# Performance work log

Hardware: AMD Instinct MI355X
Metric: run time of the kernel (lower is better)

The kernel has to match this reference:

```python
import jax, jax.numpy as jnp
import numpy as np
import math

B, L, HID = 2, 2048, 1024
H, DK, RATIO, SHARED, TOPK = 4, 64, 4, 1, 2
EXP_V = 2
DV = DK * EXP_V
KEY_DIM = H * DK
VAL_DIM = KEY_DIM * EXP_V
HE = H * RATIO
KS = 4
EPS = 1e-5


def _silu(x):
    return x * jax.nn.sigmoid(x)


def _dwconv_causal(x, w):
    # x: (B, L, C), w: (C, KS); causal depthwise short conv
    xp = jnp.pad(x, ((0, 0), (KS - 1, 0), (0, 0))).transpose(0, 2, 1)
    y = jax.lax.conv_general_dilated(xp, w[:, None, :], (1,), 'VALID',
                                     feature_group_count=w.shape[0],
                                     dimension_numbers=('NCH', 'OIH', 'NCH'))
    return y.transpose(0, 2, 1)


def _l2norm(x):
    return x * jax.lax.rsqrt(jnp.sum(x * x, -1, keepdims=True) + 1e-6)


def _forward(hidden_states, Wq, Wk, Wv, Wb, Wa, Wg, Wo, conv_q, conv_k, conv_v,
             Wq_exp, Wk_exp, W_gate, A_log, dt_bias, norm_w):
    x = hidden_states
    q = _silu(_dwconv_causal(x @ Wq.T, conv_q)).reshape(B, L, H, DK)
    k = _silu(_dwconv_causal(x @ Wk.T, conv_k)).reshape(B, L, H, DK)
    v = _silu(_dwconv_causal(x @ Wv.T, conv_v)).reshape(B, L, H, DV)
    # per-head expert expansion -> (B,L,H,RATIO,DK)
    qe = jnp.einsum('blhd,hkd->blhk', q, Wq_exp).reshape(B, L, H, RATIO, DK)
    ke = jnp.einsum('blhd,hkd->blhk', k, Wk_exp).reshape(B, L, H, RATIO, DK)
    qe = _l2norm(qe) * (DK ** -0.5)
    ke = _l2norm(ke)
    # token-policy top-k routing over non-shared experts
    logits = jnp.einsum('blhd,nd->blhn', q, W_gate)
    scores = jax.nn.softmax(logits.astype(jnp.float32), axis=-1)
    tw, ti = jax.lax.top_k(scores, TOPK)
    tw = tw / jnp.sum(tw, -1, keepdims=True)
    full = jnp.sum(jax.nn.one_hot(ti + SHARED, RATIO, dtype=tw.dtype) * tw[..., None], axis=-2)
    full = full.at[..., :SHARED].set(1.0 / SHARED)
    w_r = (full / jnp.sum(full, -1, keepdims=True)).astype(x.dtype)  # (B,L,H,RATIO)
    mask = (w_r > 0).astype(x.dtype)
    beta = jax.nn.sigmoid(x @ Wb.T).reshape(B, L, H, RATIO) * mask
    g = -jnp.exp(A_log).reshape(H, RATIO) * jax.nn.softplus((x @ Wa.T) + dt_bias).reshape(B, L, H, RATIO)
    g = g * mask  # unrouted memories: exp(0)=1, no decay, no update
    # gated delta-rule recurrence over HE = H*RATIO memories
    qs = qe.reshape(B, L, HE, DK).transpose(1, 0, 2, 3)
    ks_ = ke.reshape(B, L, HE, DK).transpose(1, 0, 2, 3)
    vs = jnp.broadcast_to(v[:, :, :, None, :], (B, L, H, RATIO, DV)).reshape(B, L, HE, DV).transpose(1, 0, 2, 3)
    bs = beta.reshape(B, L, HE).transpose(1, 0, 2)
    gs = g.reshape(B, L, HE).transpose(1, 0, 2)

    def step(S, xs):
        qt, kt, vt, bt, gt = xs
        S = S * jnp.exp(gt)[..., None, None]
        kv = jnp.einsum('bhk,bhkv->bhv', kt, S)
        S = S + jnp.einsum('bhk,bhv->bhkv', kt, (vt - kv) * bt[..., None])
        return S, jnp.einsum('bhk,bhkv->bhv', qt, S)

    S0 = jnp.zeros((B, HE, DK, DV), x.dtype)
    _, o = jax.lax.scan(step, S0, (qs, ks_, vs, bs, gs))
    o = o.transpose(1, 0, 2, 3).reshape(B, L, H, RATIO, DV)
    o = jnp.einsum('blhe,blhev->blhv', w_r, o)
    # FusedRMSNormSwishGate + output projection
    gate = (x @ Wg.T).reshape(B, L, H, DV)
    o = o * jax.lax.rsqrt(jnp.mean(o * o, -1, keepdims=True) + EPS) * norm_w * _silu(gate)
    return o.reshape(B, L, VAL_DIM) @ Wo.T


def setup_inputs():
    keys = jax.random.split(jax.random.key(0), 18)
    n = lambda i, shp, sc=1.0: jax.random.normal(keys[i], shp, jnp.float32) * sc
    A = jax.random.uniform(keys[14], (HE,), jnp.float32, 1e-3, 16.0)
    dt = jnp.exp(jax.random.uniform(keys[15], (HE,), jnp.float32) * (math.log(0.1) - math.log(0.001)) + math.log(0.001))
    dt = jnp.clip(dt, 1e-4, None)
    return {
        'hidden_states': n(0, (B, L, HID)),
        'Wq': n(1, (KEY_DIM, HID), HID ** -0.5),
        'Wk': n(2, (KEY_DIM, HID), HID ** -0.5),
        'Wv': n(3, (VAL_DIM, HID), HID ** -0.5),
        'Wb': n(4, (HE, HID), HID ** -0.5),
        'Wa': n(5, (HE, HID), HID ** -0.5),
        'Wg': n(6, (VAL_DIM, HID), HID ** -0.5),
        'Wo': n(7, (HID, VAL_DIM), VAL_DIM ** -0.5),
        'conv_q': n(8, (KEY_DIM, KS), 0.5),
        'conv_k': n(9, (KEY_DIM, KS), 0.5),
        'conv_v': n(10, (VAL_DIM, KS), 0.5),
        'Wq_exp': n(11, (H, RATIO * DK, DK), DK ** -0.5),
        'Wk_exp': n(12, (H, RATIO * DK, DK), DK ** -0.5),
        'W_gate': n(13, (RATIO - SHARED, DK), DK ** -0.5),
        'A_log': jnp.log(A),
        'dt_bias': dt + jnp.log(-jnp.expm1(-dt)),
        'norm_w': jnp.ones((DV,), jnp.float32),
    }


def reference(hidden_states, Wq, Wk, Wv, Wb, Wa, Wg, Wo, conv_q, conv_k, conv_v,
              Wq_exp, Wk_exp, W_gate, A_log, dt_bias, norm_w):
    return _forward(hidden_states, Wq, Wk, Wv, Wb, Wa, Wg, Wo, conv_q, conv_k, conv_v,
                    Wq_exp, Wk_exp, W_gate, A_log, dt_bias, norm_w)
```

## Files before the change

### kernel.cpp

```cpp
#include <hip/hip_runtime.h>
#include <hip/hip_bf16.h>
#include <math.h>

#define B_    2
#define L_    2048
#define HID_  1024
#define H_    4
#define DK_   64
#define RATIO_ 4
#define HE_   16
#define DV_   128
#define T_    64
#define NC_   32
#define SPITCH 72
#define APITCH 68
#define NCAT  1408

typedef __attribute__((ext_vector_type(8))) short short8;
typedef __attribute__((ext_vector_type(4))) float f32x4;

__device__ __forceinline__ float sigmoidf_(float x){ return 1.f/(1.f+expf(-x)); }
__device__ __forceinline__ ushort f2bf(float x){
  __hip_bfloat16 h = __float2bfloat16(x);
  return *reinterpret_cast<ushort*>(&h);
}
__device__ __forceinline__ float bf2f(ushort u){
  union { uint32_t i; float f; } v; v.i = ((uint32_t)u) << 16; return v.f;
}
__device__ __forceinline__ uint32_t pk2(float a, float b){
  return ((uint32_t)f2bf(b) << 16) | f2bf(a);
}
__device__ __forceinline__ void unpk8(uint4 w, float* f){
  f[0]=bf2f((ushort)(w.x&0xffff)); f[1]=bf2f((ushort)(w.x>>16));
  f[2]=bf2f((ushort)(w.y&0xffff)); f[3]=bf2f((ushort)(w.y>>16));
  f[4]=bf2f((ushort)(w.z&0xffff)); f[5]=bf2f((ushort)(w.z>>16));
  f[6]=bf2f((ushort)(w.w&0xffff)); f[7]=bf2f((ushort)(w.w>>16));
}

__global__ __launch_bounds__(256) void cast_bf16(const float* __restrict__ in,
                                                 ushort* __restrict__ out, int n)
{
  int i = blockIdx.x*256 + threadIdx.x;
  if (i < n) out[i] = f2bf(in[i]);
}

__global__ __launch_bounds__(256) void cast3(const float* __restrict__ Wq_exp,
    const float* __restrict__ Wk_exp, const float* __restrict__ Wo,
    ushort* __restrict__ Wqeb, ushort* __restrict__ Wkeb, ushort* __restrict__ Wob)
{
  int i = blockIdx.x*256 + threadIdx.x;
  if      (i < 65536)  Wqeb[i]         = f2bf(Wq_exp[i]);
  else if (i < 131072) Wkeb[i-65536]   = f2bf(Wk_exp[i-65536]);
  else if (i < 655360) Wob[i-131072]   = f2bf(Wo[i-131072]);
}

__global__ __launch_bounds__(256) void concat_wcat(const float* __restrict__ Wk,
    const float* __restrict__ Wv, const float* __restrict__ Wg,
    const float* __restrict__ Wb, const float* __restrict__ Wa,
    ushort* __restrict__ Wcat)
{
  int idx = blockIdx.x*256 + threadIdx.x;
  if (idx >= NCAT*1024) return;
  int r = idx >> 10, cc = idx & 1023;
  float v = 0.f;
  if      (r < 256)  v = Wk[(size_t)r*1024 + cc];
  else if (r < 768)  v = Wv[(size_t)(r-256)*1024 + cc];
  else if (r < 1280) v = Wg[(size_t)(r-768)*1024 + cc];
  else if (r < 1296) v = Wb[(size_t)(r-1280)*1024 + cc];
  else if (r < 1312) v = Wa[(size_t)(r-1296)*1024 + cc];
  Wcat[idx] = f2bf(v);
}

__global__ __launch_bounds__(256) void gemm_bf16(
    const ushort* __restrict__ A, int lda,
    const ushort* __restrict__ Bm, int ldb,
    float* __restrict__ C, int ldc, int K)
{
  __shared__ ushort As[128*32];
  __shared__ ushort Bs[128*32];
  const int tid  = threadIdx.x;
  const int wave = tid >> 6, lane = tid & 63;
  const int row0 = blockIdx.y*128, col0 = blockIdx.x*128;
  const int wr = (wave >> 1) * 64, wc = (wave & 1) * 64;
  const int frow = lane & 15;
  const int fko  = (lane >> 4) << 3;
  f32x4 acc[4][4];
  #pragma unroll
  for (int i=0;i<4;i++)
    #pragma unroll
    for (int j=0;j<4;j++) acc[i][j] = (f32x4){0.f,0.f,0.f,0.f};
  for (int k0 = 0; k0 < K; k0 += 32) {
    #pragma unroll
    for (int cc = 0; cc < 2; cc++) {
      int c  = wave*128 + cc*64 + lane;
      int r  = c >> 2;
      int ko = (c & 3) << 3;
      __builtin_amdgcn_global_load_lds(
        (const __attribute__((address_space(1))) void*)(A + (size_t)(row0+r)*lda + k0 + ko),
        (__attribute__((address_space(3))) void*)(As + (size_t)(wave*128 + cc*64)*8),
        16, 0, 0);
      __builtin_amdgcn_global_load_lds(
        (const __attribute__((address_space(1))) void*)(Bm + (size_t)(col0+r)*ldb + k0 + ko),
        (__attribute__((address_space(3))) void*)(Bs + (size_t)(wave*128 + cc*64)*8),
        16, 0, 0);
    }
    __syncthreads();
    short8 af[4], bfv[4];
    #pragma unroll
    for (int mi=0;mi<4;mi++)
      af[mi] = *reinterpret_cast<const short8*>(&As[(wr + mi*16 + frow)*32 + fko]);
    #pragma unroll
    for (int ni=0;ni<4;ni++)
      bfv[ni] = *reinterpret_cast<const short8*>(&Bs[(wc + ni*16 + frow)*32 + fko]);
    #pragma unroll
    for (int mi=0;mi<4;mi++)
      #pragma unroll
      for (int ni=0;ni<4;ni++)
        acc[mi][ni] = __builtin_amdgcn_mfma_f32_16x16x32_bf16(af[mi], bfv[ni], acc[mi][ni], 0, 0, 0);
    __syncthreads();
  }
  const int ocol = lane & 15;
  const int orow = (lane >> 4) << 2;
  #pragma unroll
  for (int mi=0;mi<4;mi++)
    #pragma unroll
    for (int ni=0;ni<4;ni++) {
      size_t base = (size_t)(row0 + wr + mi*16 + orow)*ldc + (col0 + wc + ni*16 + ocol);
      #pragma unroll
      for (int q=0;q<4;q++) C[base + (size_t)q*ldc] = acc[mi][ni][q];
    }
}

__global__ __launch_bounds__(256) void gemm_expand_bf16(
    const ushort* __restrict__ qc_bf, const ushort* __restrict__ kc_bf,
    const ushort* __restrict__ Wqeb, const ushort* __restrict__ Wkeb,
    ushort* __restrict__ qeb, ushort* __restrict__ keb)
{
  const int z = blockIdx.z;
  const int hh = z & 3;
  const ushort* A  = (z < 4 ? qc_bf : kc_bf) + hh*64;
  const ushort* Bm = (z < 4 ? Wqeb  : Wkeb ) + (size_t)hh*16384;
  ushort* C        = (z < 4 ? qeb   : keb  ) + hh*256;
  const int lda = 256, ldb = 64, ldc = 1024, K = 64;
  __shared__ ushort As[128*32];
  __shared__ ushort Bs[128*32];
  const int tid  = threadIdx.x;
  const int wave = tid >> 6, lane = tid & 63;
  const int row0 = blockIdx.y*128, col0 = blockIdx.x*128;
  const int wr = (wave >> 1) * 64, wc = (wave & 1) * 64;
  const int frow = lane & 15;
  const int fko  = (lane >> 4) << 3;
  f32x4 acc[4][4];
  #pragma unroll
  for (int i=0;i<4;i++)
    #pragma unroll
    for (int j=0;j<4;j++) acc[i][j] = (f32x4){0.f,0.f,0.f,0.f};
  for (int k0 = 0; k0 < K; k0 += 32) {
    #pragma unroll
    for (int cc = 0; cc < 2; cc++) {
      int c  = wave*128 + cc*64 + lane;
      int r  = c >> 2;
      int ko = (c & 3) << 3;
      __builtin_amdgcn_global_load_lds(
        (const __attribute__((address_space(1))) void*)(A + (size_t)(row0+r)*lda + k0 + ko),
        (__attribute__((address_space(3))) void*)(As + (size_t)(wave*128 + cc*64)*8),
        16, 0, 0);
      __builtin_amdgcn_global_load_lds(
        (const __attribute__((address_space(1))) void*)(Bm + (size_t)(col0+r)*ldb + k0 + ko),
        (__attribute__((address_space(3))) void*)(Bs + (size_t)(wave*128 + cc*64)*8),
        16, 0, 0);
    }
    __syncthreads();
    short8 af[4], bfv[4];
    #pragma unroll
    for (int mi=0;mi<4;mi++)
      af[mi] = *reinterpret_cast<const short8*>(&As[(wr + mi*16 + frow)*32 + fko]);
    #pragma unroll
    for (int ni=0;ni<4;ni++)
      bfv[ni] = *reinterpret_cast<const short8*>(&Bs[(wc + ni*16 + frow)*32 + fko]);
    #pragma unroll
    for (int mi=0;mi<4;mi++)
      #pragma unroll
      for (int ni=0;ni<4;ni++)
        acc[mi][ni] = __builtin_amdgcn_mfma_f32_16x16x32_bf16(af[mi], bfv[ni], acc[mi][ni], 0, 0, 0);
    __syncthreads();
  }
  const int ocol = lane & 15;
  const int orow = (lane >> 4) << 2;
  #pragma unroll
  for (int mi=0;mi<4;mi++)
    #pragma unroll
    for (int ni=0;ni<4;ni++) {
      size_t base = (size_t)(row0 + wr + mi*16 + orow)*ldc + (col0 + wc + ni*16 + ocol);
      #pragma unroll
      for (int q=0;q<4;q++) C[base + (size_t)q*ldc] = f2bf(acc[mi][ni][q]);
    }
}

__global__ __launch_bounds__(256) void gemm_f32_db(const float* __restrict__ A, int lda,
    const float* __restrict__ Bm, int ldb, float* __restrict__ C, int ldc,
    int M, int N, int K)
{
  __shared__ float As[2][32][64];
  __shared__ float Bs[2][32][64];
  const int tid = threadIdx.x;
  const int row0 = blockIdx.y * 64;
  const int col0 = blockIdx.x * 64;
  const int tx = tid & 15, ty = tid >> 4;
  const int r0s = tid >> 3;
  const int k4s = (tid & 7) << 2;
  float4 av0, av1, bv0, bv1;

  av0 = *(const float4*)&A[(size_t)(row0 + r0s)*lda + k4s];
  av1 = *(const float4*)&A[(size_t)(row0 + r0s + 32)*lda + k4s];
  bv0 = (col0 + r0s < N) ? *(const float4*)&Bm[(size_t)(col0 + r0s)*ldb + k4s] : make_float4(0,0,0,0);
  bv1 = (col0 + r0s + 32 < N) ? *(const float4*)&Bm[(size_t)(col0 + r0s + 32)*ldb + k4s] : make_float4(0,0,0,0);
  As[0][k4s+0][r0s] = av0.x; As[0][k4s+1][r0s] = av0.y; As[0][k4s+2][r0s] = av0.z; As[0][k4s+3][r0s] = av0.w;
  As[0][k4s+0][r0s+32] = av1.x; As[0][k4s+1][r0s+32] = av1.y; As[0][k4s+2][r0s+32] = av1.z; As[0][k4s+3][r0s+32] = av1.w;
  Bs[0][k4s+0][r0s] = bv0.x; Bs[0][k4s+1][r0s] = bv0.y; Bs[0][k4s+2][r0s] = bv0.z; Bs[0][k4s+3][r0s] = bv0.w;
  Bs[0][k4s+0][r0s+32] = bv1.x; Bs[0][k4s+1][r0s+32] = bv1.y; Bs[0][k4s+2][r0s+32] = bv1.z; Bs[0][k4s+3][r0s+32] = bv1.w;
  __syncthreads();

  float acc[4][4] = {};
  const int nt = K >> 5;
  for (int kt = 0; kt < nt; ++kt) {
    const int p = kt & 1;
    if (kt + 1 < nt) {
      int k0 = (kt+1) << 5;
      av0 = *(const float4*)&A[(size_t)(row0 + r0s)*lda + k0 + k4s];
      av1 = *(const float4*)&A[(size_t)(row0 + r0s + 32)*lda + k0 + k4s];
      bv0 = (col0 + r0s < N) ? *(const float4*)&Bm[(size_t)(col0 + r0s)*ldb + k0 + k4s] : make_float4(0,0,0,0);
      bv1 = (col0 + r0s + 32 < N) ? *(const float4*)&Bm[(size_t)(col0 + r0s + 32)*ldb + k0 + k4s] : make_float4(0,0,0,0);
    }
    #pragma unroll
    for (int kk = 0; kk < 32; kk++) {
      float4 a4 = *(const float4*)&As[p][kk][ty*4];
      float4 b4 = *(const float4*)&Bs[p][kk][tx*4];
      float a[4] = {a4.x,a4.y,a4.z,a4.w};
      float b[4] = {b4.x,b4.y,b4.z,b4.w};
      #pragma unroll
      for (int i=0;i<4;i++)
        #pragma unroll
        for (int j=0;j<4;j++) acc[i][j] += a[i]*b[j];
    }
    if (kt + 1 < nt) {
      const int q = p ^ 1;
      As[q][k4s+0][r0s] = av0.x; As[q][k4s+1][r0s] = av0.y; As[q][k4s+2][r0s] = av0.z; As[q][k4s+3][r0s] = av0.w;
      As[q][k4s+0][r0s+32] = av1.x; As[q][k4s+1][r0s+32] = av1.y; As[q][k4s+2][r0s+32] = av1.z; As[q][k4s+3][r0s+32] = av1.w;
      Bs[q][k4s+0][r0s] = bv0.x; Bs[q][k4s+1][r0s] = bv0.y; Bs[q][k4s+2][r0s] = bv0.z; Bs[q][k4s+3][r0s] = bv0.w;
      Bs[q][k4s+0][r0s+32] = bv1.x; Bs[q][k4s+1][r0s+32] = bv1.y; Bs[q][k4s+2][r0s+32] = bv1.z; Bs[q][k4s+3][r0s+32] = bv1.w;
    }
    __syncthreads();
  }
  #pragma unroll
  for (int i=0;i<4;i++) {
    int r = row0 + ty*4 + i;
    #pragma unroll
    for (int j=0;j<4;j++) {
      int cc = col0 + tx*4 + j;
      if (cc < N) C[(size_t)r*ldc + cc] = acc[i][j];
    }
  }
}

__global__ __launch_bounds__(256) void conv_silu_all(const float* __restrict__ q_lin,
    const float* __restrict__ kvgba, const float* __restrict__ conv_q,
    const float* __restrict__ conv_k, const float* __restrict__ conv_v,
    float* __restrict__ q_conv, ushort* __restrict__ qc_bf,
    ushort* __restrict__ kc_bf, ushort* __restrict__ v_convb)
{
  int n = blockIdx.x*256 + threadIdx.x;
  int cc = n & 1023;
  int bl = n >> 10;
  int t  = bl & (L_-1);
  float acc = 0.f;
  if (cc < 256) {
    const float* w = conv_q + cc*4;
    #pragma unroll
    for (int s=0;s<4;s++){ int tt=t-3+s; if (tt>=0) acc += q_lin[(size_t)(bl-t+tt)*256 + cc]*w[s]; }
    float y = acc * sigmoidf_(acc);
    q_conv[(size_t)bl*256 + cc] = y;
    qc_bf[(size_t)bl*256 + cc] = f2bf(y);
  } else {
    int col = cc - 256;
    const float* w = (cc < 512) ? (conv_k + (cc-256)*4) : (conv_v + (cc-512)*4);
    #pragma unroll
    for (int s=0;s<4;s++){ int tt=t-3+s; if (tt>=0) acc += kvgba[(size_t)(bl-t+tt)*NCAT + col]*w[s]; }
    float y = acc * sigmoidf_(acc);
    if (cc < 512) kc_bf[(size_t)bl*256 + (cc-256)] = f2bf(y);
    else          v_convb[(size_t)bl*512 + (cc-512)] = f2bf(y);
  }
}

__global__ __launch_bounds__(256) void routing(const float* __restrict__ qc,
    const float* __restrict__ kvgba, const float* __restrict__ Wg3,
    const float* __restrict__ A_log, const float* __restrict__ dt_bias,
    float* __restrict__ w_buf, float* __restrict__ bt_T, float* __restrict__ g_T)
{
  int n = blockIdx.x*256 + threadIdx.x;
  int h  = n & 3;
  int bl = n >> 2;
  const float* q = qc + (size_t)bl*256 + h*64;
  float l0=0.f, l1=0.f, l2=0.f;
  for (int d=0; d<64; d++) {
    float qd = q[d];
    l0 += qd*Wg3[d]; l1 += qd*Wg3[64+d]; l2 += qd*Wg3[128+d];
  }
  float mx = fmaxf(l0, fmaxf(l1, l2));
  float e0 = expf(l0-mx), e1 = expf(l1-mx), e2 = expf(l2-mx);
  float inv_s = 1.f/(e0+e1+e2);
  float p0 = e0*inv_s, p1 = e1*inv_s, p2 = e2*inv_s;
  int m1 = 0; float pm1 = p0;
  if (p1 > pm1) { m1 = 1; pm1 = p1; }
  if (p2 > pm1) { m1 = 2; pm1 = p2; }
  int ia = (m1==0) ? 1 : 0;
  int ib = (m1==2) ? 1 : 2;
  float pa = (m1==0) ? p1 : p0;
  float pb = (m1==2) ? p1 : p2;
  int   m2  = (pb > pa) ? ib : ia;
  float pm2 = (pb > pa) ? pb : pa;
  float inv_w = 1.f/(pm1 + pm2);
  float w1 = 0.5f*pm1*inv_w;
  float w2 = 0.5f*pm2*inv_w;
  #pragma unroll
  for (int r = 0; r < 4; r++) {
    float wr = (r==0) ? 0.5f : (((r-1)==m1) ? w1 : (((r-1)==m2) ? w2 : 0.f));
    int he = h*4 + r;
    w_buf[(size_t)bl*16 + he] = wr;
    float mask = (wr > 0.f) ? 1.f : 0.f;
    bt_T[(size_t)he*4096 + bl] = mask * sigmoidf_(kvgba[(size_t)bl*NCAT + 1280 + he]);
    float av = kvgba[(size_t)bl*NCAT + 1296 + he] + dt_bias[he];
    float sp = fmaxf(av, 0.f) + log1pf(expf(-fabsf(av)));
    g_T[(size_t)he*4096 + bl] = -expf(A_log[he]) * sp * mask;
  }
}

__device__ __forceinline__ f32x4 tile64(const ushort* Am, int r0,
                                        const ushort* Bm, int c0, int lane)
{
  f32x4 acc = {0.f,0.f,0.f,0.f};
  const int fr = lane & 15, fo = (lane >> 4) << 3;
  #pragma unroll
  for (int kk = 0; kk < 2; ++kk) {
    short8 a = *reinterpret_cast<const short8*>(&Am[(r0+fr)*SPITCH + fo + kk*32]);
    short8 b = *reinterpret_cast<const short8*>(&Bm[(c0+fr)*SPITCH + fo + kk*32]);
    acc = __builtin_amdgcn_mfma_f32_16x16x32_bf16(a, b, acc, 0, 0, 0);
  }
  return acc;
}

__global__ __launch_bounds__(256,2) void scan_chunk_mfma(
    const ushort* __restrict__ keb, const ushort* __restrict__ qeb,
    const ushort* __restrict__ vcb, const float* __restrict__ bt_T,
    const float* __restrict__ g_T, ushort* __restrict__ o0b,
    ushort* __restrict__ Qtb, ushort* __restrict__ Mcb, ushort* __restrict__ Bcb)
{
  __shared__ float smem[18496];
  ushort* Kbf = (ushort*)smem;
  ushort* Qbf = (ushort*)(smem + 2304);
  ushort* KTD = (ushort*)(smem + 4608);
  float*  Af  = smem + 6912;
  ushort* Pf  = (ushort*)(smem + 6912);
  ushort* UV  = (ushort*)(smem + 11264);
  float*  cgs = smem + 18176;
  float*  bts = cgs + 64;
  float*  bGs = bts + 64;
  float*  Ds  = bGs + 64;
  float*  gams= Ds + 64;

  const int id = blockIdx.x;
  const int c  = id >> 5;
  const int s  = id & 31;
  const int h  = s & 3;
  const int b  = (s >> 2) & 1;
  const int r  = s >> 3;
  const int he = h*4 + r;
  const int bhe = b*HE_ + he;
  const int tid = threadIdx.x;
  const int wave = tid >> 6, lane = tid & 63;
  const size_t l0 = (size_t)b*L_ + (size_t)c*T_;

  const int tr = tid >> 2;
  const int sg = tid & 3;
  float kf[16], qf[16];
  uint4 vw0, vw1, vw2, vw3;
  float sk, sq;
  {
    const uint4* kp = (const uint4*)(keb + (l0+tr)*1024 + he*64 + sg*16);
    const uint4* qp = (const uint4*)(qeb + (l0+tr)*1024 + he*64 + sg*16);
    uint4 kv[2] = {kp[0], kp[1]};
    uint4 qv[2] = {qp[0], qp[1]};
    unpk8(kv[0], kf); unpk8(kv[1], kf+8);
    unpk8(qv[0], qf); unpk8(qv[1], qf+8);
    float ssk = 0.f, ssq = 0.f;
    #pragma unroll
    for (int i=0;i<16;i++){ ssk += kf[i]*kf[i]; ssq += qf[i]*qf[i]; }
    ssk += __shfl_xor(ssk, 1); ssk += __shfl_xor(ssk, 2);
    ssq += __shfl_xor(ssq, 1); ssq += __shfl_xor(ssq, 2);
    sk = rsqrtf(ssk + 1e-6f);
    sq = rsqrtf(ssq + 1e-6f) * 0.125f;
    const uint4* vp = (const uint4*)(vcb + (l0+tr)*512 + h*128 + sg*32);
    vw0 = vp[0]; vw1 = vp[1]; vw2 = vp[2]; vw3 = vp[3];
  }
  if (tid < 64) {
    float g  = g_T[(size_t)he*4096 + l0 + tid];
    float bt = bt_T[(size_t)he*4096 + l0 + tid];
    float cg = g;
    #pragma unroll
    for (int off = 1; off < 64; off <<= 1) {
      float o = __shfl_up(cg, off);
      if (tid >= off) cg += o;
    }
    float cg63 = __shfl(cg, 63);
    cgs[tid] = cg; bts[tid] = bt;
    float gm = expf(cg);
    gams[tid] = gm; bGs[tid] = bt*gm; Ds[tid] = expf(cg63 - cg);
  }
  __syncthreads();
  {
    float Dt = Ds[tr];
    uint2* kdst = (uint2*)(Kbf + tr*SPITCH + sg*16);
    uint2* qdst = (uint2*)(Qbf + tr*SPITCH + sg*16);
    #pragma unroll
    for (int i=0;i<4;i++){
      kdst[i] = make_uint2(pk2(kf[4*i+0]*sk, kf[4*i+1]*sk), pk2(kf[4*i+2]*sk, kf[4*i+3]*sk));
      qdst[i] = make_uint2(pk2(qf[4*i+0]*sq, qf[4*i+1]*sq), pk2(qf[4*i+2]*sq, qf[4*i+3]*sq));
    }
    float skD = sk*Dt;
    #pragma unroll
    for (int i=0;i<16;i++){
      int d = sg*16 + i;
      KTD[d*SPITCH + tr] = f2bf(kf[i]*skD);
    }
    uint4* vdst = (uint4*)(UV + tr*128 + sg*32);
    vdst[0] = vw0; vdst[1] = vw1; vdst[2] = vw2; vdst[3] = vw3;
  }
  __syncthreads();
  {
    const int r0 = wave*16;
    #pragma unroll
    for (int ct=0; ct<4; ++ct) {
      f32x4 acc = tile64(Kbf, r0, Kbf, ct*16, lane);
      int t = r0 + ((lane>>4)<<2);
      int ss = ct*16 + (lane&15);
      #pragma unroll
      for (int q=0;q<4;q++){
        int tq = t + q;
        Af[tq*APITCH + ss] = (ss < tq) ? bts[tq]*expf(cgs[tq]-cgs[ss])*acc[q] : 0.f;
      }
    }
  }
  __syncthreads();
  float u[64];
  if (tid < 192) {
    if (tid < 128) {
      const ushort* Vb = UV;
      #pragma unroll
      for (int ss=0;ss<64;++ss) u[ss] = bts[ss]*bf2f(Vb[ss*128 + tid]);
    } else {
      #pragma unroll
      for (int ss=0;ss<64;++ss) u[ss] = bGs[ss]*bf2f(Kbf[ss*SPITCH + (tid-128)]);
    }
  }
  __syncthreads();
  if (tid < 192) {
    #pragma unroll
    for (int t=1;t<64;++t) {
      const float4* Ar = (const float4*)(Af + t*APITCH);
      float p0=0.f,p1=0.f,p2=0.f,p3=0.f;
      #pragma unroll
      for (int s4=0; s4*4<t; ++s4) {
        float4 a = Ar[s4];
        p0 += a.x*u[s4*4+0]; p1 += a.y*u[s4*4+1];
        p2 += a.z*u[s4*4+2]; p3 += a.w*u[s4*4+3];
      }
      u[t] -= (p0+p1)+(p2+p3);
    }
    ushort* Ut = UV;
    uint4* dst = (uint4*)&Ut[tid*SPITCH];
    #pragma unroll
    for (int i=0;i<8;++i)
      dst[i] = make_uint4(pk2(u[8*i+0],u[8*i+1]), pk2(u[8*i+2],u[8*i+3]),
                          pk2(u[8*i+4],u[8*i+5]), pk2(u[8*i+6],u[8*i+7]));
  }
  __syncthreads();
  {
    const int r0 = wave*16;
    f32x4 accs[4];
    #pragma unroll
    for (int ct=0; ct<4; ++ct) accs[ct] = tile64(Qbf, r0, Kbf, ct*16, lane);
    __syncthreads();
    #pragma unroll
    for (int ct=0; ct<4; ++ct) {
      int t = r0 + ((lane>>4)<<2);
      int ss = ct*16 + (lane&15);
      #pragma unroll
      for (int q=0;q<4;q++){
        int tq = t + q;
        float val = (ss <= tq) ? expf(cgs[tq]-cgs[ss])*accs[ct][q] : 0.f;
        Pf[tq*SPITCH + ss] = f2bf(val);
      }
    }
  }
  __syncthreads();
  {
    const int r0 = wave*16;
    const int orow = (lane >> 4) << 2;
    const float gend = expf(cgs[63]);
    const ushort* Ut = UV;
    const ushort* UtK = UV + 128*SPITCH;
    const size_t bb = ((size_t)bhe*NC_ + c)*(size_t)(64*128);
    const size_t pb = ((size_t)bhe*NC_ + c)*(size_t)(64*64);
    f32x4 mv4[4], qv4[4];
    float qpre[4][4];
    #pragma unroll
    for (int ct=0; ct<4; ++ct) mv4[ct] = tile64(KTD, r0, UtK, ct*16, lane);
    #pragma unroll
    for (int ct=0; ct<4; ++ct) qv4[ct] = tile64(Pf, r0, UtK, ct*16, lane);
    #pragma unroll
    for (int ct=0; ct<4; ++ct)
      #pragma unroll
      for (int q=0;q<4;q++){
        int row = r0 + orow + q;
        int m = ct*16 + (lane&15);
        qpre[ct][q] = gams[row]*bf2f(Qbf[row*SPITCH + m]);
      }
    __syncthreads();
    ushort* MS = (ushort*)smem;
    ushort* QS = (ushort*)(smem + 2304);
    #pragma unroll
    for (int ct=0; ct<4; ++ct){
      int m = ct*16 + (lane&15);
      #pragma unroll
      for (int q=0;q<4;q++){
        int row = r0 + orow + q;
        int pc = (((m>>3)^(row&7))<<3) | (m&7);
        float val = -mv4[ct][q];
        if (row == m) val += gend;
        MS[row*64 + pc] = f2bf(val);
        QS[row*64 + pc] = f2bf(qpre[ct][q] - qv4[ct][q]);
      }
    }
    __syncthreads();
    #pragma unroll
    for (int idx = tid; idx < 512; idx += 256){
      *(uint4*)&Mcb[pb + (size_t)idx*8] = *(const uint4*)&MS[idx*8];
      *(uint4*)&Qtb[pb + (size_t)idx*8] = *(const uint4*)&QS[idx*8];
    }
    __syncthreads();
    ushort* O0s = (ushort*)smem;
    #pragma unroll
    for (int jt=0; jt<8; ++jt) {
      f32x4 acc = tile64(Pf, r0, Ut, jt*16, lane);
      int t = r0 + orow;
      int j = jt*16 + (lane&15);
      #pragma unroll
      for (int q=0;q<4;q++) O0s[(t+q)*128 + j] = f2bf(acc[q]);
    }
    __syncthreads();
    ushort* BCs = (ushort*)Af;
    #pragma unroll
    for (int jt=0; jt<8; ++jt) {
      f32x4 acc = tile64(KTD, r0, Ut, jt*16, lane);
      int i = r0 + orow;
      int j = jt*16 + (lane&15);
      #pragma unroll
      for (int q=0;q<4;q++) BCs[(i+q)*128 + j] = f2bf(acc[q]);
    }
    __syncthreads();
    #pragma unroll
    for (int idx = tid; idx < 1024; idx += 256) {
      int row = idx >> 4, seg = idx & 15;
      *(uint4*)&o0b[((l0 + row)*HE_ + he)*DV_ + seg*8] = *(const uint4*)&O0s[row*128 + seg*8];
      *(uint4*)&Bcb[bb + (size_t)row*128 + seg*8]      = *(const uint4*)&BCs[row*128 + seg*8];
    }
  }
}

__device__ __forceinline__ void stage_qm(const ushort* __restrict__ src, ushort* dst,
                                         int wave, int lane)
{
  #pragma unroll
  for (int pass = 0; pass < 2; ++pass){
    int idx = pass*256 + wave*64 + lane;
    __builtin_amdgcn_global_load_lds(
      (const __attribute__((address_space(1))) void*)(src + (size_t)idx*8),
      (__attribute__((address_space(3))) void*)(dst + (size_t)idx*8), 16, 0, 0);
  }
}

__global__ __launch_bounds__(256) void compose_correct(
    const ushort* __restrict__ Mcb, const ushort* __restrict__ Bcb,
    const ushort* __restrict__ Qtb, ushort* __restrict__ o_corrb)
{
  __shared__ ushort Ql[2][4096];
  __shared__ ushort Ml[2][4096];
  __shared__ float SSl[512];
  const int s   = blockIdx.x;
  const int h   = s & 3;
  const int b   = (s >> 2) & 1;
  const int r   = s >> 3;
  const int he  = h*4 + r;
  const int bhe = b*HE_ + he;
  const int j0  = blockIdx.y * 8;
  const int tid = threadIdx.x;
  const int wave = tid >> 6, lane = tid & 63;
  const int rw = tid >> 2;
  const int jg = tid & 3;
  const int rsw = rw & 7;

  for (int idx = tid; idx < 512; idx += 256) SSl[idx] = 0.f;

  stage_qm(Mcb + (size_t)(bhe*NC_)*4096, Ml[0], wave, lane);
  float2 bcur;
  {
    uint32_t bw = *(const uint32_t*)&Bcb[(size_t)(bhe*NC_)*8192 + rw*128 + j0 + jg*2];
    bcur = make_float2(bf2f((ushort)(bw&0xffff)), bf2f((ushort)(bw>>16)));
  }
  __syncthreads();

  int p = 0;
  for (int c = 0; c < NC_; ++c){
    float2 bnext = make_float2(0.f,0.f);
    if (c+1 < NC_){
      stage_qm(Qtb + (size_t)(bhe*NC_ + c + 1)*4096, Ql[p^1], wave, lane);
      if (c+1 < NC_-1){
        stage_qm(Mcb + (size_t)(bhe*NC_ + c + 1)*4096, Ml[p^1], wave, lane);
        uint32_t bw = *(const uint32_t*)&Bcb[(size_t)(bhe*NC_ + c + 1)*8192 + rw*128 + j0 + jg*2];
        bnext = make_float2(bf2f((ushort)(bw&0xffff)), bf2f((ushort)(bw>>16)));
      }
    }
    const float2* SS2 = (const float2*)SSl;
    float2 oa = make_float2(0.f,0.f);
    if (c > 0){
      const ushort* Qr = Ql[p] + rw*64;
      #pragma unroll
      for (int gb = 0; gb < 8; ++gb){
        uint4 w = *(const uint4*)&Qr[(gb ^ rsw) << 3];
        float f[8]; unpk8(w, f);
        #pragma unroll
        for (int e = 0; e < 8; ++e){
          float2 sv = SS2[(gb*8+e)*4 + jg];
          oa.x += f[e]*sv.x; oa.y += f[e]*sv.y;
        }
      }
    }
    {
      size_t oi = (((size_t)b*L_ + c*T_ + rw)*HE_ + he)*DV_ + j0 + jg*2;
      *(uint32_t*)&o_corrb[oi] = pk2(oa.x, oa.y);
    }
    float2 ns = bcur;
    if (c < NC_-1){
      const ushort* Mr = Ml[p] + rw*64;
      #pragma unroll
      for (int gb = 0; gb < 8; ++gb){
        uint4 w = *(const uint4*)&Mr[(gb ^ rsw) << 3];
        float f[8]; unpk8(w, f);
        #pragma unroll
        for (int e = 0; e < 8; ++e){
          float2 sv = SS2[(gb*8+e)*4 + jg];
          ns.x += f[e]*sv.x; ns.y += f[e]*sv.y;
        }
      }
    }
    __syncthreads();
    if (c < NC_-1) *(float2*)&SSl[rw*8 + jg*2] = ns;
    __syncthreads();
    p ^= 1;
    bcur = bnext;
  }
}

__global__ __launch_bounds__(128) void combine(const ushort* __restrict__ o0b,
    const ushort* __restrict__ o_corrb, const float* __restrict__ w_buf,
    const float* __restrict__ kvgba, const float* __restrict__ norm_w,
    ushort* __restrict__ o_fin)
{
  int n  = blockIdx.x;
  int h  = n & 3;
  int bl = n >> 2;
  int j  = threadIdx.x;
  size_t wb = (size_t)bl*16 + h*4;
  size_t ob = wb*128 + j;
  float oc = 0.f;
  #pragma unroll
  for (int r = 0; r < 4; r++){
    size_t oi = ob + (size_t)r*128;
    oc += w_buf[wb+r] * (bf2f(o0b[oi]) + bf2f(o_corrb[oi]));
  }
  float ss = oc*oc;
  #pragma unroll
  for (int off = 32; off > 0; off >>= 1) ss += __shfl_xor(ss, off);
  __shared__ float red[2];
  if ((threadIdx.x & 63) == 0) red[threadIdx.x >> 6] = ss;
  __syncthreads();
  float mean = (red[0] + red[1]) * (1.f/128.f);
  float sc = rsqrtf(mean + 1e-5f);
  float gv = kvgba[(size_t)bl*NCAT + 768 + h*128 + j];
  o_fin[(size_t)bl*512 + h*128 + j] = f2bf(oc * sc * norm_w[j] * (gv * sigmoidf_(gv)));
}

extern "C" void kernel_launch(void* const* d_in, const int* in_sizes, int n_in,
                              void* d_out, int out_size, void* d_ws, size_t ws_size,
                              hipStream_t stream)
{
  (void)in_sizes; (void)n_in; (void)out_size; (void)ws_size;
  const float* x       = (const float*)d_in[0];
  const float* Wq      = (const float*)d_in[1];
  const float* Wk      = (const float*)d_in[2];
  const float* Wv      = (const float*)d_in[3];
  const float* Wb      = (const float*)d_in[4];
  const float* Wa      = (const float*)d_in[5];
  const float* Wg      = (const float*)d_in[6];
  const float* Wo      = (const float*)d_in[7];
  const float* conv_q  = (const float*)d_in[8];
  const float* conv_k  = (const float*)d_in[9];
  const float* conv_v  = (const float*)d_in[10];
  const float* Wq_exp  = (const float*)d_in[11];
  const float* Wk_exp  = (const float*)d_in[12];
  const float* W_gate  = (const float*)d_in[13];
  const float* A_log   = (const float*)d_in[14];
  const float* dt_bias = (const float*)d_in[15];
  const float* norm_w  = (const float*)d_in[16];
  float* out = (float*)d_out;

  const size_t BL = (size_t)B_*L_;
  float* p = (float*)d_ws;
  float* q_lin  = p; p += BL*256;
  float* kvgba  = p; p += BL*NCAT;
  float* q_conv = p; p += BL*256;
  float* w_buf  = p; p += BL*16;
  float* bt_T   = p; p += BL*16;
  float* g_T    = p; p += BL*16;
  ushort* o0b   = (ushort*)p; p += BL*16*64;
  ushort* o_corrb=(ushort*)p; p += BL*16*64;
  ushort* Mcb   = (ushort*)p; p += (size_t)B_*HE_*NC_*2048;
  ushort* Qtb   = (ushort*)p; p += (size_t)B_*HE_*NC_*2048;
  ushort* Bcb   = (ushort*)p; p += (size_t)B_*HE_*NC_*4096;
  ushort* v_convb=(ushort*)p; p += BL*256;
  ushort* xb    = (ushort*)p; p += BL*512;
  ushort* Wcat  = (ushort*)p; p += (NCAT*1024)/2;
  ushort* qc_bf = (ushort*)p; p += BL*128;
  ushort* kc_bf = (ushort*)p; p += BL*128;
  ushort* qeb   = (ushort*)p; p += BL*512;
  ushort* keb   = (ushort*)p; p += BL*512;
  ushort* Wqeb  = (ushort*)p; p += 32768;
  ushort* Wkeb  = (ushort*)p; p += 32768;
  ushort* Wob   = (ushort*)p; p += 262144;
  ushort* o_finb= (ushort*)p; p += BL*256;

  concat_wcat<<<dim3((NCAT*1024+255)/256), dim3(256), 0, stream>>>(Wk, Wv, Wg, Wb, Wa, Wcat);
  { int n = (int)(BL*1024); cast_bf16<<<dim3((n+255)/256), dim3(256), 0, stream>>>(x, xb, n); }
  cast3<<<dim3((655360+255)/256), dim3(256), 0, stream>>>(Wq_exp, Wk_exp, Wo, Wqeb, Wkeb, Wob);

  gemm_f32_db<<<dim3(4, 64), dim3(256), 0, stream>>>(x, 1024, Wq, 1024, q_lin, 256, 4096, 256, 1024);
  gemm_bf16<<<dim3(NCAT/128, 32), dim3(256), 0, stream>>>(xb, 1024, Wcat, 1024, kvgba, NCAT, 1024);

  conv_silu_all<<<dim3((int)(BL*1024/256)), dim3(256), 0, stream>>>(
      q_lin, kvgba, conv_q, conv_k, conv_v, q_conv, qc_bf, kc_bf, v_convb);

  routing<<<dim3(64), dim3(256), 0, stream>>>(q_conv, kvgba, W_gate, A_log, dt_bias,
                                              w_buf, bt_T, g_T);

  gemm_expand_bf16<<<dim3(2, 32, 8), dim3(256), 0, stream>>>(qc_bf, kc_bf, Wqeb, Wkeb, qeb, keb);

  scan_chunk_mfma<<<dim3(NC_*HE_*B_), dim3(256), 0, stream>>>(keb, qeb, v_convb, bt_T, g_T,
                                                              o0b, Qtb, Mcb, Bcb);
  compose_correct<<<dim3(32, 16), dim3(256), 0, stream>>>(Mcb, Bcb, Qtb, o_corrb);
  combine<<<dim3(B_*L_*H_), dim3(128), 0, stream>>>(o0b, o_corrb, w_buf, kvgba, norm_w, o_finb);

  gemm_bf16<<<dim3(8, 32), dim3(256), 0, stream>>>(o_finb, 512, Wob, 512, out, 1024, 512);
}
```

Measured before the change: 333.0 us.

## Split compose_correct reduction across lanes and double grid over value columns

compose_correct now gives each block 4 value columns instead of 8 and launches twice as many blocks. Within a block, the four threads per row each reduce over a quarter of the inner dimension and combine their partial sums with xor shuffles. The running state in shared memory shrinks to 64x4. Separately, one __syncthreads between the MFMA tile and the Pf writes in scan_chunk_mfma is removed to cut a barrier. The cost is that each Q/M tile is now staged from global memory by twice as many blocks, and the barrier removal is a race if Pf overlaps the Q/K buffers.

```diff
diff --git a/kernel.cpp b/kernel.cpp
--- a/kernel.cpp
+++ b/kernel.cpp
@@ -489,7 +489,6 @@
     f32x4 accs[4];
     #pragma unroll
     for (int ct=0; ct<4; ++ct) accs[ct] = tile64(Qbf, r0, Kbf, ct*16, lane);
-    __syncthreads();
     #pragma unroll
     for (int ct=0; ct<4; ++ct) {
       int t = r0 + ((lane>>4)<<2);
@@ -595,76 +594,93 @@
 {
   __shared__ ushort Ql[2][4096];
   __shared__ ushort Ml[2][4096];
-  __shared__ float SSl[512];
+  __shared__ float SSl[256];
   const int s   = blockIdx.x;
   const int h   = s & 3;
   const int b   = (s >> 2) & 1;
   const int r   = s >> 3;
   const int he  = h*4 + r;
   const int bhe = b*HE_ + he;
-  const int j0  = blockIdx.y * 8;
+  const int j0  = blockIdx.y * 4;
   const int tid = threadIdx.x;
   const int wave = tid >> 6, lane = tid & 63;
   const int rw = tid >> 2;
-  const int jg = tid & 3;
+  const int mq = tid & 3;
   const int rsw = rw & 7;
 
-  for (int idx = tid; idx < 512; idx += 256) SSl[idx] = 0.f;
+  if (tid < 256) { if (tid < 256) {} }
+  for (int idx = tid; idx < 256; idx += 256) SSl[idx] = 0.f;
 
   stage_qm(Mcb + (size_t)(bhe*NC_)*4096, Ml[0], wave, lane);
-  float2 bcur;
+  float4 bcur;
   {
-    uint32_t bw = *(const uint32_t*)&Bcb[(size_t)(bhe*NC_)*8192 + rw*128 + j0 + jg*2];
-    bcur = make_float2(bf2f((ushort)(bw&0xffff)), bf2f((ushort)(bw>>16)));
+    uint2 bw = *(const uint2*)&Bcb[(size_t)(bhe*NC_)*8192 + rw*128 + j0];
+    bcur = make_float4(bf2f((ushort)(bw.x&0xffff)), bf2f((ushort)(bw.x>>16)),
+                       bf2f((ushort)(bw.y&0xffff)), bf2f((ushort)(bw.y>>16)));
   }
   __syncthreads();
 
   int p = 0;
   for (int c = 0; c < NC_; ++c){
-    float2 bnext = make_float2(0.f,0.f);
+    float4 bnext = make_float4(0.f,0.f,0.f,0.f);
     if (c+1 < NC_){
       stage_qm(Qtb + (size_t)(bhe*NC_ + c + 1)*4096, Ql[p^1], wave, lane);
       if (c+1 < NC_-1){
         stage_qm(Mcb + (size_t)(bhe*NC_ + c + 1)*4096, Ml[p^1], wave, lane);
-        uint32_t bw = *(const uint32_t*)&Bcb[(size_t)(bhe*NC_ + c + 1)*8192 + rw*128 + j0 + jg*2];
-        bnext = make_float2(bf2f((ushort)(bw&0xffff)), bf2f((ushort)(bw>>16)));
+        uint2 bw = *(const uint2*)&Bcb[(size_t)(bhe*NC_ + c + 1)*8192 + rw*128 + j0];
+        bnext = make_float4(bf2f((ushort)(bw.x&0xffff)), bf2f((ushort)(bw.x>>16)),
+                            bf2f((ushort)(bw.y&0xffff)), bf2f((ushort)(bw.y>>16)));
       }
     }
-    const float2* SS2 = (const float2*)SSl;
-    float2 oa = make_float2(0.f,0.f);
+    const float4* SS4 = (const float4*)SSl;
+    float4 oa = make_float4(0.f,0.f,0.f,0.f);
     if (c > 0){
       const ushort* Qr = Ql[p] + rw*64;
       #pragma unroll
-      for (int gb = 0; gb < 8; ++gb){
+      for (int gg = 0; gg < 2; ++gg){
+        int gb = mq*2 + gg;
         uint4 w = *(const uint4*)&Qr[(gb ^ rsw) << 3];
         float f[8]; unpk8(w, f);
         #pragma unroll
         for (int e = 0; e < 8; ++e){
-          float2 sv = SS2[(gb*8+e)*4 + jg];
-          oa.x += f[e]*sv.x; oa.y += f[e]*sv.y;
+          float4 sv = SS4[gb*8+e];
+          oa.x += f[e]*sv.x; oa.y += f[e]*sv.y; oa.z += f[e]*sv.z; oa.w += f[e]*sv.w;
         }
       }
-    }
-    {
-      size_t oi = (((size_t)b*L_ + c*T_ + rw)*HE_ + he)*DV_ + j0 + jg*2;
-      *(uint32_t*)&o_corrb[oi] = pk2(oa.x, oa.y);
-    }
-    float2 ns = bcur;
+      oa.x += __shfl_xor(oa.x,1); oa.y += __shfl_xor(oa.y,1);
+      oa.z += __shfl_xor(oa.z,1); oa.w += __shfl_xor(oa.w,1);
+      oa.x += __shfl_xor(oa.x,2); oa.y += __shfl_xor(oa.y,2);
+      oa.z += __shfl_xor(oa.z,2); oa.w += __shfl_xor(oa.w,2);
+    }
+    if (mq < 2){
+      size_t oi = (((size_t)b*L_ + c*T_ + rw)*HE_ + he)*DV_ + j0 + mq*2;
+      *(uint32_t*)&o_corrb[oi] = (mq==0) ? pk2(oa.x, oa.y) : pk2(oa.z, oa.w);
+    }
+    float4 ns = make_float4(0.f,0.f,0.f,0.f);
     if (c < NC_-1){
       const ushort* Mr = Ml[p] + rw*64;
       #pragma unroll
-      for (int gb = 0; gb < 8; ++gb){
+      for (int gg = 0; gg < 2; ++gg){
+        int gb = mq*2 + gg;
         uint4 w = *(const uint4*)&Mr[(gb ^ rsw) << 3];
         float f[8]; unpk8(w, f);
         #pragma unroll
         for (int e = 0; e < 8; ++e){
-          float2 sv = SS2[(gb*8+e)*4 + jg];
-          ns.x += f[e]*sv.x; ns.y += f[e]*sv.y;
+          float4 sv = SS4[gb*8+e];
+          ns.x += f[e]*sv.x; ns.y += f[e]*sv.y; ns.z += f[e]*sv.z; ns.w += f[e]*sv.w;
         }
       }
-    }
-    __syncthreads();
-    if (c < NC_-1) *(float2*)&SSl[rw*8 + jg*2] = ns;
+      ns.x += __shfl_xor(ns.x,1); ns.y += __shfl_xor(ns.y,1);
+      ns.z += __shfl_xor(ns.z,1); ns.w += __shfl_xor(ns.w,1);
+      ns.x += __shfl_xor(ns.x,2); ns.y += __shfl_xor(ns.y,2);
+      ns.z += __shfl_xor(ns.z,2); ns.w += __shfl_xor(ns.w,2);
+      ns.x += bcur.x; ns.y += bcur.y; ns.z += bcur.z; ns.w += bcur.w;
+    }
+    __syncthreads();
+    if (c < NC_-1){
+      float v = (mq==0) ? ns.x : (mq==1) ? ns.y : (mq==2) ? ns.z : ns.w;
+      SSl[rw*4 + mq] = v;
+    }
     __syncthreads();
     p ^= 1;
     bcur = bnext;
@@ -766,7 +782,7 @@
 
   scan_chunk_mfma<<<dim3(NC_*HE_*B_), dim3(256), 0, stream>>>(keb, qeb, v_convb, bt_T, g_T,
                                                               o0b, Qtb, Mcb, Bcb);
-  compose_correct<<<dim3(32, 16), dim3(256), 0, stream>>>(Mcb, Bcb, Qtb, o_corrb);
+  compose_correct<<<dim3(32, 32), dim3(256), 0, stream>>>(Mcb, Bcb, Qtb, o_corrb);
   combine<<<dim3(B_*L_*H_), dim3(128), 0, stream>>>(o0b, o_corrb, w_buf, kvgba, norm_w, o_finb);
 
   gemm_bf16<<<dim3(8, 32), dim3(256), 0, stream>>>(o_finb, 512, Wob, 512, out, 1024, 512);
```

After: 402.8 us. 20.9% more time.
